# Performance work log

Hardware: AMD Instinct MI355X
Metric: run time of the kernel (lower is better)

The kernel has to match this reference:

```python
import jax, jax.numpy as jnp
import numpy as np

BINS = 10

def setup_inputs() -> dict:
    key = jax.random.key(0)
    k1, k2 = jax.random.split(key)
    N, C = 262144, 80
    pred = jax.random.normal(k1, (N, C), dtype=jnp.float32)
    target = jax.random.randint(k2, (N, C), 0, 2, dtype=jnp.int32)
    return {"pred": pred, "target": target}


def _ghmc_loss(pred, target):
    # NOTE: faithful to the original torch code, which applies sigmoid to pred
    # and then feeds that *through binary_cross_entropy_with_logits* (i.e. the
    # sigmoid output is treated as logits -- a double sigmoid quirk we preserve).
    z = jax.nn.sigmoid(pred)                      # [N, C] "logits" fed to BCE-with-logits
    t = target.astype(z.dtype)                    # [N, C]
    # gradient magnitude, detached like pred.detach() in torch
    g = jnp.abs(jax.lax.stop_gradient(z) - t)     # in [0, 1]
    # label_weight is overwritten with ones in the original forward, so every
    # element is valid: tot = N * C.
    tot = jnp.asarray(z.size, dtype=z.dtype)

    # uniform bins: edges[i] = i/BINS, last edge nudged by 1e-6 so g == 1 lands
    # in the last bin -> equivalent to floor(g*BINS) clipped to BINS-1.
    idx = jnp.clip((g * BINS).astype(jnp.int32), 0, BINS - 1)   # [N, C]
    counts = jax.ops.segment_sum(
        jnp.ones((z.size,), dtype=z.dtype), idx.reshape(-1), num_segments=BINS
    )                                                            # [BINS]
    n_nonempty = jnp.sum(counts > 0).astype(z.dtype)
    per_bin_w = jnp.where(counts > 0, tot / jnp.maximum(counts, 1.0), 0.0)  # [BINS]
    weights = per_bin_w[idx] / jnp.maximum(n_nonempty, 1.0)      # [N, C]
    weights = jax.lax.stop_gradient(weights)

    # BCE-with-logits(z, t) = softplus(z) - t*z (numerically stable)
    bce = jax.nn.softplus(z) - t * z
    return jnp.sum(weights * bce) / tot


def reference(pred, target):
    return _ghmc_loss(pred, target)
```

## Files before the change

### kernel.cpp

```cpp
#include <hip/hip_runtime.h>


#define NBINS  10
#define GRID1  2048
#define BLOCK1 256

typedef float vf4 __attribute__((ext_vector_type(4)));
typedef int   vi4 __attribute__((ext_vector_type(4)));

__global__ __launch_bounds__(BLOCK1) void ghmc_pass1(
    const vf4* __restrict__ pred4,
    const vi4* __restrict__ targ4,
    float* __restrict__ partial_s,
    int*   __restrict__ partial_c,
    int nvec4)
{
    __shared__ float sred[BLOCK1 / 64][NBINS];
    __shared__ int   cred[BLOCK1 / 64][NBINS];

    float s[NBINS];
#pragma unroll
    for (int b = 0; b < NBINS; ++b) s[b] = 0.0f;
    unsigned long long cnt = 0;

    const int idx    = blockIdx.x * BLOCK1 + threadIdx.x;
    const int stride = GRID1 * BLOCK1;

    auto elem = [&](float x, int t) {
        float tf = (float)t;
        float e  = __expf(-x);
        float z  = __builtin_amdgcn_rcpf(1.0f + e);
        float g  = fabsf(z - tf);
        int   bi = (int)(g * 10.0f);
        bi = bi > (NBINS - 1) ? (NBINS - 1) : bi;
        float bce = __logf(1.0f + __expf(z)) - tf * z;
#pragma unroll
        for (int b = 0; b < NBINS; ++b)
            s[b] += (bi == b) ? bce : 0.0f;
        cnt += 1ull << (6 * bi);
    };

    int i = idx;
    for (; i + stride < nvec4; i += 2 * stride) {
        vf4 p0 = pred4[i];
        vi4 t0 = targ4[i];
        vf4 p1 = pred4[i + stride];
        vi4 t1 = targ4[i + stride];
        elem(p0[0], t0[0]); elem(p0[1], t0[1]); elem(p0[2], t0[2]); elem(p0[3], t0[3]);
        elem(p1[0], t1[0]); elem(p1[1], t1[1]); elem(p1[2], t1[2]); elem(p1[3], t1[3]);
    }
    if (i < nvec4) {
        vf4 p0 = pred4[i];
        vi4 t0 = targ4[i];
        elem(p0[0], t0[0]); elem(p0[1], t0[1]); elem(p0[2], t0[2]); elem(p0[3], t0[3]);
    }

    int c[NBINS];
#pragma unroll
    for (int b = 0; b < NBINS; ++b) c[b] = (int)((cnt >> (6 * b)) & 63ull);

#pragma unroll
    for (int b = 0; b < NBINS; ++b) {
#pragma unroll
        for (int off = 32; off > 0; off >>= 1) {
            s[b] += __shfl_down(s[b], off, 64);
            c[b] += __shfl_down(c[b], off, 64);
        }
    }

    const int wave = threadIdx.x >> 6;
    if ((threadIdx.x & 63) == 0) {
#pragma unroll
        for (int b = 0; b < NBINS; ++b) { sred[wave][b] = s[b]; cred[wave][b] = c[b]; }
    }
    __syncthreads();
    if (threadIdx.x < NBINS) {
        int b = threadIdx.x;
        partial_s[b * GRID1 + blockIdx.x] = sred[0][b] + sred[1][b] + sred[2][b] + sred[3][b];
        partial_c[b * GRID1 + blockIdx.x] = cred[0][b] + cred[1][b] + cred[2][b] + cred[3][b];
    }
}

#define BLOCK2 1024

__global__ __launch_bounds__(BLOCK2) void ghmc_pass2(
    const float* __restrict__ partial_s,
    const int*   __restrict__ partial_c,
    float* __restrict__ out,
    int nblocks)
{
    double as[NBINS];
    int    ac[NBINS];
#pragma unroll
    for (int b = 0; b < NBINS; ++b) { as[b] = 0.0; ac[b] = 0; }

    for (int j = threadIdx.x; j < nblocks; j += BLOCK2) {
#pragma unroll
        for (int b = 0; b < NBINS; ++b) {
            as[b] += (double)partial_s[b * nblocks + j];
            ac[b] += partial_c[b * nblocks + j];
        }
    }

#pragma unroll
    for (int b = 0; b < NBINS; ++b) {
#pragma unroll
        for (int off = 32; off > 0; off >>= 1) {
            as[b] += __shfl_down(as[b], off, 64);
            ac[b] += __shfl_down(ac[b], off, 64);
        }
    }

    __shared__ double sds[BLOCK2 / 64][NBINS];
    __shared__ int    sdc[BLOCK2 / 64][NBINS];
    int wave = threadIdx.x >> 6;
    if ((threadIdx.x & 63) == 0) {
#pragma unroll
        for (int b = 0; b < NBINS; ++b) { sds[wave][b] = as[b]; sdc[wave][b] = ac[b]; }
    }
    __syncthreads();

    if (threadIdx.x == 0) {
        int nn = 0;
        double acc = 0.0;
#pragma unroll
        for (int b = 0; b < NBINS; ++b) {
            double sb = 0.0;
            int    cb = 0;
#pragma unroll
            for (int w = 0; w < BLOCK2 / 64; ++w) { sb += sds[w][b]; cb += sdc[w][b]; }
            if (cb > 0) { nn += 1; acc += sb / (double)cb; }
        }
        out[0] = (float)(acc / (double)(nn > 0 ? nn : 1));
    }
}

extern "C" void kernel_launch(void* const* d_in, const int* in_sizes, int n_in,
                              void* d_out, int out_size, void* d_ws, size_t ws_size,
                              hipStream_t stream)
{
    const float* pred = (const float*)d_in[0];
    const int*   targ = (const int*)d_in[1];
    float*       out  = (float*)d_out;

    const int n     = in_sizes[0];
    const int nvec4 = n / 4;

    float* partial_s = (float*)d_ws;
    int*   partial_c = (int*)((char*)d_ws + GRID1 * NBINS * sizeof(float));

    ghmc_pass1<<<GRID1, BLOCK1, 0, stream>>>(
        (const vf4*)pred, (const vi4*)targ, partial_s, partial_c, nvec4);

    ghmc_pass2<<<1, BLOCK2, 0, stream>>>(partial_s, partial_c, out, GRID1);
}
```

Measured before the change: 202.9 us.

## Fuse final reduction into main kernel via last-block ticket and software-pipeline loads

Merges the second reduction kernel into the first: each block writes its partials, takes an atomic ticket, and the last block to finish performs the final cross-block reduction and writes the loss. The main loop is also restructured to prefetch the next vector while computing the current one, instead of processing two strided vectors per iteration. This aims to remove a separate kernel launch and its serialization gap, at the cost of a memset launch for the ticket and a last-block tail. The count packing of 6 bits per bin still holds because each thread handles at most a few vectors.

```diff
diff --git a/kernel.cpp b/kernel.cpp
--- a/kernel.cpp
+++ b/kernel.cpp
@@ -8,15 +8,18 @@
 typedef float vf4 __attribute__((ext_vector_type(4)));
 typedef int   vi4 __attribute__((ext_vector_type(4)));
 
-__global__ __launch_bounds__(BLOCK1) void ghmc_pass1(
+__global__ __launch_bounds__(BLOCK1) void ghmc_fused(
     const vf4* __restrict__ pred4,
     const vi4* __restrict__ targ4,
     float* __restrict__ partial_s,
     int*   __restrict__ partial_c,
+    unsigned int* __restrict__ ticket,
+    float* __restrict__ out,
     int nvec4)
 {
     __shared__ float sred[BLOCK1 / 64][NBINS];
     __shared__ int   cred[BLOCK1 / 64][NBINS];
+    __shared__ unsigned int is_last;
 
     float s[NBINS];
 #pragma unroll
@@ -41,18 +44,16 @@
     };
 
     int i = idx;
-    for (; i + stride < nvec4; i += 2 * stride) {
-        vf4 p0 = pred4[i];
-        vi4 t0 = targ4[i];
-        vf4 p1 = pred4[i + stride];
-        vi4 t1 = targ4[i + stride];
-        elem(p0[0], t0[0]); elem(p0[1], t0[1]); elem(p0[2], t0[2]); elem(p0[3], t0[3]);
-        elem(p1[0], t1[0]); elem(p1[1], t1[1]); elem(p1[2], t1[2]); elem(p1[3], t1[3]);
-    }
     if (i < nvec4) {
-        vf4 p0 = pred4[i];
-        vi4 t0 = targ4[i];
-        elem(p0[0], t0[0]); elem(p0[1], t0[1]); elem(p0[2], t0[2]); elem(p0[3], t0[3]);
+        vf4 p = pred4[i];
+        vi4 t = targ4[i];
+        for (int j = i + stride; j < nvec4; j += stride) {
+            vf4 pn = pred4[j];
+            vi4 tn = targ4[j];
+            elem(p[0], t[0]); elem(p[1], t[1]); elem(p[2], t[2]); elem(p[3], t[3]);
+            p = pn; t = tn;
+        }
+        elem(p[0], t[0]); elem(p[1], t[1]); elem(p[2], t[2]); elem(p[3], t[3]);
     }
 
     int c[NBINS];
@@ -79,26 +80,27 @@
         partial_s[b * GRID1 + blockIdx.x] = sred[0][b] + sred[1][b] + sred[2][b] + sred[3][b];
         partial_c[b * GRID1 + blockIdx.x] = cred[0][b] + cred[1][b] + cred[2][b] + cred[3][b];
     }
-}
 
-#define BLOCK2 1024
+    if (threadIdx.x == 0) {
+        __threadfence();
+        unsigned int my = atomicAdd(ticket, 1u);
+        is_last = (my == (unsigned int)(GRID1 - 1)) ? 1u : 0u;
+    }
+    __syncthreads();
+    if (!is_last) return;
 
-__global__ __launch_bounds__(BLOCK2) void ghmc_pass2(
-    const float* __restrict__ partial_s,
-    const int*   __restrict__ partial_c,
-    float* __restrict__ out,
-    int nblocks)
-{
+    __threadfence();
+
     double as[NBINS];
     int    ac[NBINS];
 #pragma unroll
     for (int b = 0; b < NBINS; ++b) { as[b] = 0.0; ac[b] = 0; }
 
-    for (int j = threadIdx.x; j < nblocks; j += BLOCK2) {
+    for (int j = threadIdx.x; j < GRID1; j += BLOCK1) {
 #pragma unroll
         for (int b = 0; b < NBINS; ++b) {
-            as[b] += (double)partial_s[b * nblocks + j];
-            ac[b] += partial_c[b * nblocks + j];
+            as[b] += (double)partial_s[b * GRID1 + j];
+            ac[b] += partial_c[b * GRID1 + j];
         }
     }
 
@@ -111,9 +113,8 @@
         }
     }
 
-    __shared__ double sds[BLOCK2 / 64][NBINS];
-    __shared__ int    sdc[BLOCK2 / 64][NBINS];
-    int wave = threadIdx.x >> 6;
+    __shared__ double sds[BLOCK1 / 64][NBINS];
+    __shared__ int    sdc[BLOCK1 / 64][NBINS];
     if ((threadIdx.x & 63) == 0) {
 #pragma unroll
         for (int b = 0; b < NBINS; ++b) { sds[wave][b] = as[b]; sdc[wave][b] = ac[b]; }
@@ -128,7 +129,7 @@
             double sb = 0.0;
             int    cb = 0;
 #pragma unroll
-            for (int w = 0; w < BLOCK2 / 64; ++w) { sb += sds[w][b]; cb += sdc[w][b]; }
+            for (int w = 0; w < BLOCK1 / 64; ++w) { sb += sds[w][b]; cb += sdc[w][b]; }
             if (cb > 0) { nn += 1; acc += sb / (double)cb; }
         }
         out[0] = (float)(acc / (double)(nn > 0 ? nn : 1));
@@ -146,11 +147,12 @@
     const int n     = in_sizes[0];
     const int nvec4 = n / 4;
 
-    float* partial_s = (float*)d_ws;
-    int*   partial_c = (int*)((char*)d_ws + GRID1 * NBINS * sizeof(float));
+    float*        partial_s = (float*)d_ws;
+    int*          partial_c = (int*)((char*)d_ws + GRID1 * NBINS * sizeof(float));
+    unsigned int* ticket    = (unsigned int*)((char*)d_ws + 2 * GRID1 * NBINS * sizeof(float));
 
-    ghmc_pass1<<<GRID1, BLOCK1, 0, stream>>>(
-        (const vf4*)pred, (const vi4*)targ, partial_s, partial_c, nvec4);
+    hipMemsetAsync(ticket, 0, sizeof(unsigned int), stream);
 
-    ghmc_pass2<<<1, BLOCK2, 0, stream>>>(partial_s, partial_c, out, GRID1);
+    ghmc_fused<<<GRID1, BLOCK1, 0, stream>>>(
+        (const vf4*)pred, (const vi4*)targ, partial_s, partial_c, ticket, out, nvec4);
 }
```

Result: slower. 304.6 us (+50.1%).

## Split GHM-C loss into count pass and weighted-sum pass with precomputed bin weights

Applied to the files above, without the earlier changes.

Replaces the single pass that kept ten per-bin BCE accumulators with two passes: one that only counts bin membership, and one that reduces the global counts into a per-bin weight table and accumulates a single weighted sum. It also switches to native exp2/log2 intrinsics. The aim is to remove the per-element ten-way select/accumulate and the register pressure it causes. In exchange the inputs are read twice and the sigmoid is recomputed, and every block redundantly reduces the count partials.

```diff
diff --git a/kernel.cpp b/kernel.cpp
--- a/kernel.cpp
+++ b/kernel.cpp
@@ -8,36 +8,151 @@
 typedef float vf4 __attribute__((ext_vector_type(4)));
 typedef int   vi4 __attribute__((ext_vector_type(4)));
 
-__global__ __launch_bounds__(BLOCK1) void ghmc_pass1(
+#if __has_builtin(__builtin_amdgcn_exp2f)
+__device__ __forceinline__ float nexp2(float a) { return __builtin_amdgcn_exp2f(a); }
+#else
+__device__ __forceinline__ float nexp2(float a) { return __expf(a * 0.69314718055994531f); }
+#endif
+#if __has_builtin(__builtin_amdgcn_logf)
+__device__ __forceinline__ float nlog2(float a) { return __builtin_amdgcn_logf(a); }
+#else
+__device__ __forceinline__ float nlog2(float a) { return __logf(a) * 1.44269504088896341f; }
+#endif
+
+#define LOG2E 1.44269504088896341f
+#define LN2   0.69314718055994531f
+
+__global__ __launch_bounds__(BLOCK1) void ghmc_counts(
     const vf4* __restrict__ pred4,
     const vi4* __restrict__ targ4,
-    float* __restrict__ partial_s,
-    int*   __restrict__ partial_c,
+    int* __restrict__ partial_c,
     int nvec4)
 {
-    __shared__ float sred[BLOCK1 / 64][NBINS];
-    __shared__ int   cred[BLOCK1 / 64][NBINS];
-
-    float s[NBINS];
-#pragma unroll
-    for (int b = 0; b < NBINS; ++b) s[b] = 0.0f;
+    __shared__ int cred[BLOCK1 / 64][NBINS];
+
     unsigned long long cnt = 0;
 
     const int idx    = blockIdx.x * BLOCK1 + threadIdx.x;
     const int stride = GRID1 * BLOCK1;
 
+    auto binof = [&](float x, int t) -> int {
+        float tf = (float)t;
+        float z  = __builtin_amdgcn_rcpf(1.0f + nexp2(-x * LOG2E));
+        float g  = fabsf(z - tf);
+        int   bi = (int)(g * 10.0f);
+        return bi > (NBINS - 1) ? (NBINS - 1) : bi;
+    };
+
+    int i = idx;
+    for (; i + stride < nvec4; i += 2 * stride) {
+        vf4 p0 = pred4[i];
+        vi4 t0 = targ4[i];
+        vf4 p1 = pred4[i + stride];
+        vi4 t1 = targ4[i + stride];
+        cnt += 1ull << (6 * binof(p0[0], t0[0]));
+        cnt += 1ull << (6 * binof(p0[1], t0[1]));
+        cnt += 1ull << (6 * binof(p0[2], t0[2]));
+        cnt += 1ull << (6 * binof(p0[3], t0[3]));
+        cnt += 1ull << (6 * binof(p1[0], t1[0]));
+        cnt += 1ull << (6 * binof(p1[1], t1[1]));
+        cnt += 1ull << (6 * binof(p1[2], t1[2]));
+        cnt += 1ull << (6 * binof(p1[3], t1[3]));
+    }
+    if (i < nvec4) {
+        vf4 p0 = pred4[i];
+        vi4 t0 = targ4[i];
+        cnt += 1ull << (6 * binof(p0[0], t0[0]));
+        cnt += 1ull << (6 * binof(p0[1], t0[1]));
+        cnt += 1ull << (6 * binof(p0[2], t0[2]));
+        cnt += 1ull << (6 * binof(p0[3], t0[3]));
+    }
+
+    int c[NBINS];
+#pragma unroll
+    for (int b = 0; b < NBINS; ++b) c[b] = (int)((cnt >> (6 * b)) & 63ull);
+
+#pragma unroll
+    for (int b = 0; b < NBINS; ++b) {
+#pragma unroll
+        for (int off = 32; off > 0; off >>= 1)
+            c[b] += __shfl_down(c[b], off, 64);
+    }
+
+    const int wave = threadIdx.x >> 6;
+    if ((threadIdx.x & 63) == 0) {
+#pragma unroll
+        for (int b = 0; b < NBINS; ++b) cred[wave][b] = c[b];
+    }
+    __syncthreads();
+    if (threadIdx.x < NBINS) {
+        int b = threadIdx.x;
+        partial_c[b * GRID1 + blockIdx.x] = cred[0][b] + cred[1][b] + cred[2][b] + cred[3][b];
+    }
+}
+
+__global__ __launch_bounds__(BLOCK1) void ghmc_wsum(
+    const vf4* __restrict__ pred4,
+    const vi4* __restrict__ targ4,
+    const int* __restrict__ partial_c,
+    float* __restrict__ partial_f,
+    int nvec4)
+{
+    __shared__ int   credb[BLOCK1 / 64][NBINS];
+    __shared__ int   ctot[NBINS];
+    __shared__ float wtab[NBINS];
+    __shared__ float fred[BLOCK1 / 64];
+
+    {
+        int cb[NBINS];
+#pragma unroll
+        for (int b = 0; b < NBINS; ++b) cb[b] = 0;
+        for (int k = threadIdx.x; k < GRID1; k += BLOCK1) {
+#pragma unroll
+            for (int b = 0; b < NBINS; ++b)
+                cb[b] += partial_c[b * GRID1 + k];
+        }
+#pragma unroll
+        for (int b = 0; b < NBINS; ++b) {
+#pragma unroll
+            for (int off = 32; off > 0; off >>= 1)
+                cb[b] += __shfl_down(cb[b], off, 64);
+        }
+        const int wave = threadIdx.x >> 6;
+        if ((threadIdx.x & 63) == 0) {
+#pragma unroll
+            for (int b = 0; b < NBINS; ++b) credb[wave][b] = cb[b];
+        }
+        __syncthreads();
+        if (threadIdx.x < NBINS) {
+            int b = threadIdx.x;
+            ctot[b] = credb[0][b] + credb[1][b] + credb[2][b] + credb[3][b];
+        }
+        __syncthreads();
+        if (threadIdx.x < NBINS) {
+            int nn = 0;
+#pragma unroll
+            for (int k = 0; k < NBINS; ++k) nn += (ctot[k] > 0) ? 1 : 0;
+            int cb0 = ctot[threadIdx.x];
+            wtab[threadIdx.x] = (cb0 > 0)
+                ? (float)(1.0 / ((double)cb0 * (double)nn)) : 0.0f;
+        }
+        __syncthreads();
+    }
+
+    float acc = 0.0f;
+
+    const int idx    = blockIdx.x * BLOCK1 + threadIdx.x;
+    const int stride = GRID1 * BLOCK1;
+
     auto elem = [&](float x, int t) {
         float tf = (float)t;
-        float e  = __expf(-x);
-        float z  = __builtin_amdgcn_rcpf(1.0f + e);
+        float z  = __builtin_amdgcn_rcpf(1.0f + nexp2(-x * LOG2E));
         float g  = fabsf(z - tf);
         int   bi = (int)(g * 10.0f);
         bi = bi > (NBINS - 1) ? (NBINS - 1) : bi;
-        float bce = __logf(1.0f + __expf(z)) - tf * z;
-#pragma unroll
-        for (int b = 0; b < NBINS; ++b)
-            s[b] += (bi == b) ? bce : 0.0f;
-        cnt += 1ull << (6 * bi);
+        float sp = nlog2(1.0f + nexp2(z * LOG2E)) * LN2;
+        float bce = sp - tf * z;
+        acc += wtab[bi] * bce;
     };
 
     int i = idx;
@@ -55,84 +170,36 @@
         elem(p0[0], t0[0]); elem(p0[1], t0[1]); elem(p0[2], t0[2]); elem(p0[3], t0[3]);
     }
 
-    int c[NBINS];
-#pragma unroll
-    for (int b = 0; b < NBINS; ++b) c[b] = (int)((cnt >> (6 * b)) & 63ull);
-
-#pragma unroll
-    for (int b = 0; b < NBINS; ++b) {
-#pragma unroll
-        for (int off = 32; off > 0; off >>= 1) {
-            s[b] += __shfl_down(s[b], off, 64);
-            c[b] += __shfl_down(c[b], off, 64);
-        }
-    }
-
+#pragma unroll
+    for (int off = 32; off > 0; off >>= 1)
+        acc += __shfl_down(acc, off, 64);
     const int wave = threadIdx.x >> 6;
-    if ((threadIdx.x & 63) == 0) {
-#pragma unroll
-        for (int b = 0; b < NBINS; ++b) { sred[wave][b] = s[b]; cred[wave][b] = c[b]; }
-    }
+    if ((threadIdx.x & 63) == 0) fred[wave] = acc;
     __syncthreads();
-    if (threadIdx.x < NBINS) {
-        int b = threadIdx.x;
-        partial_s[b * GRID1 + blockIdx.x] = sred[0][b] + sred[1][b] + sred[2][b] + sred[3][b];
-        partial_c[b * GRID1 + blockIdx.x] = cred[0][b] + cred[1][b] + cred[2][b] + cred[3][b];
-    }
-}
-
-#define BLOCK2 1024
-
-__global__ __launch_bounds__(BLOCK2) void ghmc_pass2(
-    const float* __restrict__ partial_s,
-    const int*   __restrict__ partial_c,
+    if (threadIdx.x == 0)
+        partial_f[blockIdx.x] = fred[0] + fred[1] + fred[2] + fred[3];
+}
+
+__global__ __launch_bounds__(BLOCK1) void ghmc_final(
+    const float* __restrict__ partial_f,
     float* __restrict__ out,
     int nblocks)
 {
-    double as[NBINS];
-    int    ac[NBINS];
-#pragma unroll
-    for (int b = 0; b < NBINS; ++b) { as[b] = 0.0; ac[b] = 0; }
-
-    for (int j = threadIdx.x; j < nblocks; j += BLOCK2) {
-#pragma unroll
-        for (int b = 0; b < NBINS; ++b) {
-            as[b] += (double)partial_s[b * nblocks + j];
-            ac[b] += partial_c[b * nblocks + j];
-        }
-    }
-
-#pragma unroll
-    for (int b = 0; b < NBINS; ++b) {
-#pragma unroll
-        for (int off = 32; off > 0; off >>= 1) {
-            as[b] += __shfl_down(as[b], off, 64);
-            ac[b] += __shfl_down(ac[b], off, 64);
-        }
-    }
-
-    __shared__ double sds[BLOCK2 / 64][NBINS];
-    __shared__ int    sdc[BLOCK2 / 64][NBINS];
-    int wave = threadIdx.x >> 6;
-    if ((threadIdx.x & 63) == 0) {
-#pragma unroll
-        for (int b = 0; b < NBINS; ++b) { sds[wave][b] = as[b]; sdc[wave][b] = ac[b]; }
-    }
+    __shared__ double dred[BLOCK1 / 64];
+
+    double a = 0.0;
+    for (int j = threadIdx.x; j < nblocks; j += BLOCK1)
+        a += (double)partial_f[j];
+
+#pragma unroll
+    for (int off = 32; off > 0; off >>= 1)
+        a += __shfl_down(a, off, 64);
+
+    const int wave = threadIdx.x >> 6;
+    if ((threadIdx.x & 63) == 0) dred[wave] = a;
     __syncthreads();
-
-    if (threadIdx.x == 0) {
-        int nn = 0;
-        double acc = 0.0;
-#pragma unroll
-        for (int b = 0; b < NBINS; ++b) {
-            double sb = 0.0;
-            int    cb = 0;
-#pragma unroll
-            for (int w = 0; w < BLOCK2 / 64; ++w) { sb += sds[w][b]; cb += sdc[w][b]; }
-            if (cb > 0) { nn += 1; acc += sb / (double)cb; }
-        }
-        out[0] = (float)(acc / (double)(nn > 0 ? nn : 1));
-    }
+    if (threadIdx.x == 0)
+        out[0] = (float)(dred[0] + dred[1] + dred[2] + dred[3]);
 }
 
 extern "C" void kernel_launch(void* const* d_in, const int* in_sizes, int n_in,
@@ -146,11 +213,14 @@
     const int n     = in_sizes[0];
     const int nvec4 = n / 4;
 
-    float* partial_s = (float*)d_ws;
-    int*   partial_c = (int*)((char*)d_ws + GRID1 * NBINS * sizeof(float));
-
-    ghmc_pass1<<<GRID1, BLOCK1, 0, stream>>>(
-        (const vf4*)pred, (const vi4*)targ, partial_s, partial_c, nvec4);
-
-    ghmc_pass2<<<1, BLOCK2, 0, stream>>>(partial_s, partial_c, out, GRID1);
-}
+    int*   partial_c = (int*)d_ws;
+    float* partial_f = (float*)((char*)d_ws + NBINS * GRID1 * sizeof(int));
+
+    ghmc_counts<<<GRID1, BLOCK1, 0, stream>>>(
+        (const vf4*)pred, (const vi4*)targ, partial_c, nvec4);
+
+    ghmc_wsum<<<GRID1, BLOCK1, 0, stream>>>(
+        (const vf4*)pred, (const vi4*)targ, partial_c, partial_f, nvec4);
+
+    ghmc_final<<<1, BLOCK1, 0, stream>>>(partial_f, out, GRID1);
+}
```

New measurement: 215.0 us. 1.06x slower.
